# Kernel optimization log

Measured on AMD Instinct MI355X. Metric: run time of the kernel, lower is better.

## Reference

```python
import jax, jax.numpy as jnp
import numpy as np

# Dims (match init_kwargs)
B, N, D_MODEL = 64, 64, 512
D_STATE = 512
D_ATT = D_MODEL
H, W, C, K = 128, 128, 16, 5
T = 32  # num_steps
HALF = K // 2


def _lin(key, out_d, in_d):
    kw, kb = jax.random.split(key)
    w = jax.random.normal(kw, (out_d, in_d), jnp.float32) * 0.02
    b = jax.random.normal(kb, (out_d,), jnp.float32) * 0.02
    return w, b


def setup_inputs() -> dict:
    key = jax.random.key(0)
    ks = jax.random.split(key, 12)
    token_reps = jax.random.normal(ks[0], (B, N, D_MODEL), jnp.float32)
    global_rep = jax.random.normal(ks[1], (B, D_MODEL), jnp.float32)
    attention_mask = jnp.ones((B, N), jnp.int32)
    w_init, b_init = _lin(ks[2], D_STATE, D_MODEL)
    wq, bq = _lin(ks[3], D_ATT, D_STATE)
    wk, bk = _lin(ks[4], D_ATT, D_MODEL)
    wv, bv = _lin(ks[5], D_ATT, D_MODEL)
    gru_in = D_ATT + D_MODEL
    w_ih, b_ih = _lin(ks[6], 3 * D_STATE, gru_in)
    w_hh, b_hh = _lin(ks[7], 3 * D_STATE, D_STATE)
    w_write, b_write = _lin(ks[8], C * K * K, D_STATE + D_ATT)
    w_loc, b_loc = _lin(ks[9], 3, D_STATE + D_ATT + D_MODEL)
    return dict(token_reps=token_reps, global_rep=global_rep, attention_mask=attention_mask,
                w_init=w_init, b_init=b_init, wq=wq, bq=bq, wk=wk, bk=bk, wv=wv, bv=bv,
                w_ih=w_ih, b_ih=b_ih, w_hh=w_hh, b_hh=b_hh,
                w_write=w_write, b_write=b_write, w_loc=w_loc, b_loc=b_loc)


def _forward(token_reps, global_rep, attention_mask,
             w_init, b_init, wq, bq, wk, bk, wv, bv,
             w_ih, b_ih, w_hh, b_hh, w_write, b_write, w_loc, b_loc):
    Bv = token_reps.shape[0]
    # Precompute keys/values (constant over steps)
    k_tok = token_reps @ wk.T + bk  # [B,N,d_att]
    v_tok = token_reps @ wv.T + bv  # [B,N,d_att]
    invalid = attention_mask == 0

    s0 = jnp.tanh(global_rep @ w_init.T + b_init)  # [B,d_state]
    # Padded canvas (NHWC): full KxK patches always fit; crop at the end
    # reproduces the torch clipped-window write exactly.
    canvas0 = jnp.zeros((Bv, H + 2 * HALF, W + 2 * HALF, C), jnp.float32)
    b_idx = jnp.arange(Bv)
    koff = jnp.arange(K)

    def step(carry, _):
        s, canvas_p = carry
        q = s @ wq.T + bq  # [B,d_att]
        scores = jnp.einsum('bd,bnd->bn', q, k_tok)
        scores = jnp.where(invalid, -1e9, scores)
        alpha = jax.nn.softmax(scores, axis=-1)
        r = jnp.einsum('bn,bnd->bd', alpha, v_tok)  # [B,d_att]
        # GRUCell (torch gate order r,z,n)
        x = jnp.concatenate([r, global_rep], axis=-1)
        gi = x @ w_ih.T + b_ih
        gh = s @ w_hh.T + b_hh
        ir, iz, inn = jnp.split(gi, 3, axis=-1)
        hr, hz, hn = jnp.split(gh, 3, axis=-1)
        rg = jax.nn.sigmoid(ir + hr)
        zg = jax.nn.sigmoid(iz + hz)
        ng = jnp.tanh(inn + rg * hn)
        s_new = (1.0 - zg) * ng + zg * s
        # Write patch
        patch = (jnp.concatenate([s_new, r], axis=-1) @ w_write.T + b_write)
        patch = patch.reshape(Bv, C, K, K).transpose(0, 2, 3, 1)  # [B,K,K,C]
        loc = jnp.concatenate([s_new, r, global_rep], axis=-1) @ w_loc.T + b_loc
        cx = jnp.tanh(loc[:, 0])
        cy = jnp.tanh(loc[:, 1])
        j = jnp.clip(jnp.round(0.5 * (cx + 1.0) * (W - 1)), 0, W - 1).astype(jnp.int32)
        i = jnp.clip(jnp.round(0.5 * (cy + 1.0) * (H - 1)), 0, H - 1).astype(jnp.int32)
        # padded coords: top-left of window in padded canvas is (i, j)
        rows = i[:, None] + koff  # [B,K]
        cols = j[:, None] + koff  # [B,K]
        canvas_p = canvas_p.at[b_idx[:, None, None], rows[:, :, None], cols[:, None, :]].add(patch)
        return (s_new, canvas_p), None

    (_, canvas_p), _ = jax.lax.scan(step, (s0, canvas0), None, length=T)
    canvas = canvas_p[:, HALF:HALF + H, HALF:HALF + W, :].transpose(0, 3, 1, 2)  # [B,C,H,W]
    return canvas


def reference(token_reps, global_rep, attention_mask,
              w_init, b_init, wq, bq, wk, bk, wv, bv,
              w_ih, b_ih, w_hh, b_hh, w_write, b_write, w_loc, b_loc):
    return _forward(token_reps, global_rep, attention_mask,
                    w_init, b_init, wq, bq, wk, bk, wv, bv,
                    w_ih, b_ih, w_hh, b_hh, w_write, b_write, w_loc, b_loc)
```

## Files before the change

kernel.cpp:

```cpp
#include <hip/hip_runtime.h>

#define BB 64
#define DD 512
#define TT 32

__device__ __forceinline__ float dot4(const float4 a, const float4 b) {
  return a.x * b.x + a.y * b.y + a.z * b.z + a.w * b.w;
}

__device__ __forceinline__ void cst(float* p, float v) {
  __hip_atomic_store(p, v, __ATOMIC_RELAXED, __HIP_MEMORY_SCOPE_AGENT);
}

__global__ void vecs_k(const float* __restrict__ wq, const float* __restrict__ bk,
                       const float* __restrict__ wk, const float* __restrict__ bq,
                       float* __restrict__ kqb, float* __restrict__ wkbq,
                       float* __restrict__ bqbk, unsigned* __restrict__ bar) {
  const int tid = threadIdx.x, bz = blockIdx.x;
  if (bz < 2) {
    const int d = bz * 256 + tid;
    float s = 0.f;
    for (int e = 0; e < DD; ++e) s += wq[e * DD + d] * bk[e];
    kqb[d] = s;
  } else {
    const int k = (bz - 2) * 256 + tid;
    float s = 0.f;
    for (int e = 0; e < DD; ++e) s += bq[e] * wk[e * DD + k];
    wkbq[k] = s;
    if (bz == 2 && tid == 0) {
      float t2 = 0.f;
      for (int e = 0; e < DD; ++e) t2 += bq[e] * bk[e];
      *bqbk = t2;
    }
    if (bz == 3) {
      if (tid < 16)
        __hip_atomic_store(bar + tid * 64, 0u, __ATOMIC_RELAXED, __HIP_MEMORY_SCOPE_AGENT);
      __hip_atomic_store(bar + 1024 + tid * 32, 0u, __ATOMIC_RELAXED, __HIP_MEMORY_SCOPE_AGENT);
    }
  }
}

__global__ __launch_bounds__(256) void gemm128_k(
    const float* __restrict__ A, int lda, int a_trans,
    const float* __restrict__ B, int ldb, int boff, int b_trans,
    const float* __restrict__ bias, float* __restrict__ C, long c_stride_z, int ldc,
    int kfrom, int klen, int act) {
  __shared__ __align__(16) float As[16][132];
  __shared__ __align__(16) float Bs[16][68];
  const int tid = threadIdx.x;
  const int tx = tid & 15, ty = tid >> 4;
  const int m0 = blockIdx.x * 128, n0 = blockIdx.y * 64;
  const int kbase = kfrom + blockIdx.z * klen;
  float* Ce = C + (long)blockIdx.z * c_stride_z;
  float acc[8][4];
#pragma unroll
  for (int i = 0; i < 8; ++i)
#pragma unroll
    for (int j = 0; j < 4; ++j) acc[i][j] = 0.f;

  for (int k0 = kbase; k0 < kbase + klen; k0 += 16) {
    if (!a_trans) {
      const int row = tid >> 1, half = tid & 1;
      const float* ap = A + (long)(m0 + row) * lda + k0 + half * 8;
      const float4 a0 = *(const float4*)ap;
      const float4 a1 = *(const float4*)(ap + 4);
      const int kb = half * 8;
      As[kb + 0][row] = a0.x; As[kb + 1][row] = a0.y; As[kb + 2][row] = a0.z; As[kb + 3][row] = a0.w;
      As[kb + 4][row] = a1.x; As[kb + 5][row] = a1.y; As[kb + 6][row] = a1.z; As[kb + 7][row] = a1.w;
    } else {
      const int kk = tid >> 4, mseg = tid & 15;
      const float* ap = A + (long)(k0 + kk) * lda + m0 + mseg * 8;
      *(float4*)&As[kk][mseg * 8] = *(const float4*)ap;
      *(float4*)&As[kk][mseg * 8 + 4] = *(const float4*)(ap + 4);
    }
    if (!b_trans) {
      const int n = tid >> 2, q = tid & 3;
      const float4 b0 = *(const float4*)(B + (long)(n0 + n) * ldb + boff + k0 + q * 4);
      Bs[q * 4 + 0][n] = b0.x; Bs[q * 4 + 1][n] = b0.y; Bs[q * 4 + 2][n] = b0.z; Bs[q * 4 + 3][n] = b0.w;
    } else {
      const int kk = tid >> 4, nq = tid & 15;
      *(float4*)&Bs[kk][nq * 4] = *(const float4*)(B + (long)(k0 + kk) * ldb + boff + n0 + nq * 4);
    }
    __syncthreads();
#pragma unroll
    for (int kk = 0; kk < 16; ++kk) {
      const float4 a0 = *(const float4*)&As[kk][ty * 8];
      const float4 a1 = *(const float4*)&As[kk][ty * 8 + 4];
      const float4 b0 = *(const float4*)&Bs[kk][tx * 4];
      const float am[8] = {a0.x, a0.y, a0.z, a0.w, a1.x, a1.y, a1.z, a1.w};
#pragma unroll
      for (int i = 0; i < 8; ++i) {
        acc[i][0] += am[i] * b0.x; acc[i][1] += am[i] * b0.y;
        acc[i][2] += am[i] * b0.z; acc[i][3] += am[i] * b0.w;
      }
    }
    __syncthreads();
  }
  float4 bv = make_float4(0.f, 0.f, 0.f, 0.f);
  if (bias) bv = *(const float4*)(bias + n0 + tx * 4);
#pragma unroll
  for (int i = 0; i < 8; ++i) {
    const int m = m0 + ty * 8 + i;
    float4 v = make_float4(acc[i][0] + bv.x, acc[i][1] + bv.y, acc[i][2] + bv.z, acc[i][3] + bv.w);
    if (act == 1) { v.x = tanhf(v.x); v.y = tanhf(v.y); v.z = tanhf(v.z); v.w = tanhf(v.w); }
    *(float4*)&Ce[(long)m * ldc + n0 + tx * 4] = v;
  }
}

__global__ __launch_bounds__(256) void gemm128_dual_k(
    const float* __restrict__ A,
    const float* __restrict__ B0, const float* __restrict__ bias0, float* __restrict__ C0,
    const float* __restrict__ B1, const float* __restrict__ bias1, float* __restrict__ C1) {
  __shared__ __align__(16) float As[16][132];
  __shared__ __align__(16) float Bs[16][68];
  const int tid = threadIdx.x;
  const int tx = tid & 15, ty = tid >> 4;
  const int m0 = blockIdx.x * 128, n0 = blockIdx.y * 64;
  const float* B = blockIdx.z ? B1 : B0;
  const float* bias = blockIdx.z ? bias1 : bias0;
  float* C = blockIdx.z ? C1 : C0;
  float acc[8][4];
#pragma unroll
  for (int i = 0; i < 8; ++i)
#pragma unroll
    for (int j = 0; j < 4; ++j) acc[i][j] = 0.f;

  for (int k0 = 0; k0 < 512; k0 += 16) {
    {
      const int row = tid >> 1, half = tid & 1;
      const float* ap = A + (long)(m0 + row) * 512 + k0 + half * 8;
      const float4 a0 = *(const float4*)ap;
      const float4 a1 = *(const float4*)(ap + 4);
      const int kb = half * 8;
      As[kb + 0][row] = a0.x; As[kb + 1][row] = a0.y; As[kb + 2][row] = a0.z; As[kb + 3][row] = a0.w;
      As[kb + 4][row] = a1.x; As[kb + 5][row] = a1.y; As[kb + 6][row] = a1.z; As[kb + 7][row] = a1.w;
    }
    {
      const int n = tid >> 2, q = tid & 3;
      const float4 b0 = *(const float4*)(B + (long)(n0 + n) * 512 + k0 + q * 4);
      Bs[q * 4 + 0][n] = b0.x; Bs[q * 4 + 1][n] = b0.y; Bs[q * 4 + 2][n] = b0.z; Bs[q * 4 + 3][n] = b0.w;
    }
    __syncthreads();
#pragma unroll
    for (int kk = 0; kk < 16; ++kk) {
      const float4 a0 = *(const float4*)&As[kk][ty * 8];
      const float4 a1 = *(const float4*)&As[kk][ty * 8 + 4];
      const float4 b0 = *(const float4*)&Bs[kk][tx * 4];
      const float am[8] = {a0.x, a0.y, a0.z, a0.w, a1.x, a1.y, a1.z, a1.w};
#pragma unroll
      for (int i = 0; i < 8; ++i) {
        acc[i][0] += am[i] * b0.x; acc[i][1] += am[i] * b0.y;
        acc[i][2] += am[i] * b0.z; acc[i][3] += am[i] * b0.w;
      }
    }
    __syncthreads();
  }
  const float4 bvv = *(const float4*)(bias + n0 + tx * 4);
#pragma unroll
  for (int i = 0; i < 8; ++i) {
    const int m = m0 + ty * 8 + i;
    float4 v = make_float4(acc[i][0] + bvv.x, acc[i][1] + bvv.y, acc[i][2] + bvv.z, acc[i][3] + bvv.w);
    *(float4*)&C[(long)m * 512 + n0 + tx * 4] = v;
  }
}

__global__ void combine4_k(const float* __restrict__ p, float* __restrict__ out) {
  const int i = blockIdx.x * blockDim.x + threadIdx.x;
  const float4 a = ((const float4*)p)[i];
  const float4 b = ((const float4*)p)[i + 65536];
  const float4 c = ((const float4*)p)[i + 131072];
  const float4 d = ((const float4*)p)[i + 196608];
  ((float4*)out)[i] = make_float4(a.x + b.x + c.x + d.x, a.y + b.y + c.y + d.y,
                                  a.z + b.z + c.z + d.z, a.w + b.w + c.w + d.w);
}

__global__ __launch_bounds__(256) void gemm_k(
    const float* __restrict__ A, int lda, int a_trans,
    const float* __restrict__ B, int ldb, int boff, int b_trans,
    const float* __restrict__ bias,
    float* __restrict__ C, int ldc, int M, int N, int K, int act) {
  __shared__ __align__(16) float As2[32][68];
  __shared__ __align__(16) float Bs2[32][68];
  const int tid = threadIdx.x;
  const int tx = tid & 15, ty = tid >> 4;
  const int m0 = blockIdx.x * 64, n0 = blockIdx.y * 64;
  float acc[4][4] = {};
  for (int k0 = 0; k0 < K; k0 += 32) {
    {
      const int r = tid >> 2, cg2 = (tid & 3) * 8;
      const float* ap = A + (long)(m0 + r) * lda + k0 + cg2;
      const float4 a0 = *(const float4*)ap;
      const float4 a1 = *(const float4*)(ap + 4);
      As2[cg2 + 0][r] = a0.x; As2[cg2 + 1][r] = a0.y; As2[cg2 + 2][r] = a0.z; As2[cg2 + 3][r] = a0.w;
      As2[cg2 + 4][r] = a1.x; As2[cg2 + 5][r] = a1.y; As2[cg2 + 6][r] = a1.z; As2[cg2 + 7][r] = a1.w;
    }
    {
      const int r = tid >> 2, cg2 = (tid & 3) * 8;
      float4 b0 = make_float4(0.f, 0.f, 0.f, 0.f);
      float4 b1 = make_float4(0.f, 0.f, 0.f, 0.f);
      if (n0 + r < N) {
        const float* bp = B + (long)(n0 + r) * ldb + boff + k0 + cg2;
        b0 = *(const float4*)bp;
        b1 = *(const float4*)(bp + 4);
      }
      Bs2[cg2 + 0][r] = b0.x; Bs2[cg2 + 1][r] = b0.y; Bs2[cg2 + 2][r] = b0.z; Bs2[cg2 + 3][r] = b0.w;
      Bs2[cg2 + 4][r] = b1.x; Bs2[cg2 + 5][r] = b1.y; Bs2[cg2 + 6][r] = b1.z; Bs2[cg2 + 7][r] = b1.w;
    }
    __syncthreads();
#pragma unroll
    for (int kk = 0; kk < 32; ++kk) {
      const float4 av = *(const float4*)&As2[kk][ty * 4];
      const float4 bv = *(const float4*)&Bs2[kk][tx * 4];
      acc[0][0] += av.x * bv.x; acc[0][1] += av.x * bv.y; acc[0][2] += av.x * bv.z; acc[0][3] += av.x * bv.w;
      acc[1][0] += av.y * bv.x; acc[1][1] += av.y * bv.y; acc[1][2] += av.y * bv.z; acc[1][3] += av.y * bv.w;
      acc[2][0] += av.z * bv.x; acc[2][1] += av.z * bv.y; acc[2][2] += av.z * bv.z; acc[2][3] += av.z * bv.w;
      acc[3][0] += av.w * bv.x; acc[3][1] += av.w * bv.y; acc[3][2] += av.w * bv.z; acc[3][3] += av.w * bv.w;
    }
    __syncthreads();
  }
#pragma unroll
  for (int i = 0; i < 4; ++i) {
    const int m = m0 + ty * 4 + i;
#pragma unroll
    for (int j = 0; j < 4; ++j) {
      const int n = n0 + tx * 4 + j;
      if (n < N) {
        float v = acc[i][j] + (bias ? bias[n] : 0.f);
        if (act == 1) v = tanhf(v);
        C[(long)m * ldc + n] = v;
      }
    }
  }
}

__device__ __forceinline__ void grid_barrier(unsigned* __restrict__ bar, unsigned gen) {
  __syncthreads();
  const int blk = blockIdx.x, tid = threadIdx.x;
  unsigned* gctr = bar;
  unsigned* rel = bar + 1024;
  if (blk == 0) {
    if (tid == 0)
      __hip_atomic_fetch_add(gctr, 1u, __ATOMIC_RELAXED, __HIP_MEMORY_SCOPE_AGENT);
    if (tid < 16) {
      while (__hip_atomic_load(gctr + tid * 64, __ATOMIC_RELAXED, __HIP_MEMORY_SCOPE_AGENT) < gen * 16u)
        __builtin_amdgcn_s_sleep(1);
    }
    __syncthreads();
    __hip_atomic_store(rel + tid * 32, gen, __ATOMIC_RELAXED, __HIP_MEMORY_SCOPE_AGENT);
  } else {
    if (tid == 0) {
      __hip_atomic_fetch_add(gctr + (blk >> 4) * 64, 1u, __ATOMIC_RELAXED, __HIP_MEMORY_SCOPE_AGENT);
      while (__hip_atomic_load(rel + blk * 32, __ATOMIC_RELAXED, __HIP_MEMORY_SCOPE_AGENT) < gen)
        __builtin_amdgcn_s_sleep(1);
    }
  }
  __syncthreads();
}

__global__ __launch_bounds__(256, 1) void loop_k(
    const float* __restrict__ ktil, const float* __restrict__ cbn,
    const float* __restrict__ vt, const float* __restrict__ locg,
    float* __restrict__ sbuf, float* __restrict__ rbuf,
    const float* __restrict__ w_write, const float* __restrict__ b_write,
    const float* __restrict__ w_loc, const int* __restrict__ amask,
    float* __restrict__ patchbuf, float* __restrict__ locbuf,
    const float* __restrict__ gig, const float* __restrict__ w_ih,
    const float* __restrict__ w_hh, const float* __restrict__ b_hh,
    unsigned* __restrict__ bar) {
  __shared__ __align__(16) float smem[10048];
  __shared__ __align__(16) float wpl[12288];
  float* sm_act = smem;
  float* sm_val = smem + 9216;
  float* sm_sc  = smem + 9408;
  float* sm_s   = smem;
  float* sm_r   = smem + 4608;
  float* sm_g   = smem + 9216;

  const int blk = blockIdx.x, tid = threadIdx.x, lane = tid & 63;
  const bool is_attn = (blk < 64);
  const bool is_patch = (blk >= 64) && (blk < 224);
  unsigned nsync = 0;

  int p_rg = 0, p_bg = 0;
  if (is_patch) {
    const int g = blk - 64;
    p_bg = g & 3; p_rg = g >> 2;
    for (int idx = tid; idx < 3072; idx += 256) {
      const int rho = idx >> 8, f4 = idx & 255;
      const int col = f4 << 2;
      const int cc2 = col >> 5, jj = (col >> 2) & 7;
      const int dcol = (cc2 << 5) | ((jj ^ (cc2 & 7)) << 2);
      const float* src = (rho < 10) ? (w_write + (long)(p_rg * 10 + rho) * 1024 + col)
                                    : (w_loc + (long)(rho - 10) * 1536 + col);
      *(float4*)(wpl + rho * 1024 + dcol) = *(const float4*)src;
    }
  }

  float4 wg[3][8];
  const int g_dg = blk & 63, g_bg = blk >> 6;
  {
    const int c = tid & 15, sl = tid >> 4;
#pragma unroll
    for (int i = 0; i < 3; ++i) {
      const int rho = sl * 3 + i;
      const float* wsrc;
      if (rho < 24) {
        const int g2 = rho >> 3, di = rho & 7;
        wsrc = w_ih + (long)(g2 * 512 + g_dg * 8 + di) * 1024 + c * 32;
      } else {
        const int rh = rho - 24, g2 = rh >> 3, di = rh & 7;
        wsrc = w_hh + (long)(g2 * 512 + g_dg * 8 + di) * 512 + c * 32;
      }
#pragma unroll
      for (int j = 0; j < 8; ++j) wg[i][j] = *(const float4*)(wsrc + 4 * j);
    }
  }
  __syncthreads();

  for (int t = 0; t <= TT; ++t) {
    const float* s_cur = sbuf + (long)t * (BB * DD);
    float* r_cur = rbuf + (long)t * (BB * DD);
    const float* r_prev = r_cur - BB * DD;

    if (is_attn) {
      if (t < TT) {
        const int b = blk, wrp = tid >> 6;
        const float* sb = s_cur + (long)b * DD;
        const float4 sva = *(const float4*)(sb + lane * 8);
        const float4 svb = *(const float4*)(sb + lane * 8 + 4);
        for (int h8 = 0; h8 < 2; ++h8) {
          const float* kbase = ktil + ((long)(b * 64 + wrp * 16 + h8 * 8)) * DD + lane * 8;
          float4 ka[8], kb2[8];
#pragma unroll
          for (int i = 0; i < 8; ++i) {
            ka[i] = *(const float4*)(kbase + (long)i * DD);
            kb2[i] = *(const float4*)(kbase + (long)i * DD + 4);
          }
#pragma unroll
          for (int i = 0; i < 8; ++i) {
            float p = dot4(ka[i], sva) + dot4(kb2[i], svb);
#pragma unroll
            for (int off = 32; off; off >>= 1) p += __shfl_xor(p, off);
            if (lane == 0) {
              const int n = wrp * 16 + h8 * 8 + i;
              float sc = p + cbn[b * 64 + n];
              if (amask[b * 64 + n] == 0) sc = -1e9f;
              sm_sc[n] = sc;
            }
          }
        }
        __syncthreads();
        if (tid < 64) {
          const float v = sm_sc[tid];
          float m = v;
#pragma unroll
          for (int off = 32; off; off >>= 1) m = fmaxf(m, __shfl_xor(m, off));
          const float e = expf(v - m);
          float l2 = e;
#pragma unroll
          for (int off = 32; off; off >>= 1) l2 += __shfl_xor(l2, off);
          sm_sc[tid] = e / l2;
        }
        __syncthreads();
        float rx = 0.f, ry = 0.f;
        const float* vb = vt + (long)b * 64 * DD + (tid << 1);
        for (int n0 = 0; n0 < 64; n0 += 8) {
          float2 vv[8];
#pragma unroll
          for (int i = 0; i < 8; ++i)
            vv[i] = *(const float2*)(vb + (long)(n0 + i) * DD);
#pragma unroll
          for (int i = 0; i < 8; ++i) {
            const float a = sm_sc[n0 + i];
            rx = fmaf(a, vv[i].x, rx);
            ry = fmaf(a, vv[i].y, ry);
          }
        }
        cst(r_cur + (long)b * DD + (tid << 1), rx);
        cst(r_cur + (long)b * DD + (tid << 1) + 1, ry);
      }
    } else if (is_patch) {
      if (t >= 1) {
        const int c = tid & 31, sl = tid >> 5;
        const int tr = sl & 3, bgsub = sl >> 2;
        for (int h = 0; h < 2; ++h) {
          __syncthreads();
          {
            const int b_i8 = tid >> 5, l = tid & 31;
            const int b = p_bg * 16 + h * 8 + b_i8;
            const float* sp = s_cur + (long)b * DD + l * 16;
            const float* rp = r_prev + (long)b * DD + l * 16;
            float* dsd = sm_act + b_i8 * 1152 + (l >> 1) * 36 + (l & 1) * 16;
            float* drd = sm_act + b_i8 * 1152 + (16 + (l >> 1)) * 36 + (l & 1) * 16;
#pragma unroll
            for (int jj = 0; jj < 4; ++jj) {
              *(float4*)(dsd + 4 * jj) = *(const float4*)(sp + 4 * jj);
              *(float4*)(drd + 4 * jj) = *(const float4*)(rp + 4 * jj);
            }
          }
          __syncthreads();
          float4 wreg[3][8];
#pragma unroll
          for (int i = 0; i < 3; ++i) {
            const float* wrow = wpl + (tr * 3 + i) * 1024 + (c << 5);
#pragma unroll
            for (int j = 0; j < 8; ++j)
              wreg[i][j] = *(const float4*)(wrow + ((j ^ (c & 7)) << 2));
          }
          for (int bi = 0; bi < 4; ++bi) {
            const int bl = bgsub * 4 + bi;
            const int babs = p_bg * 16 + h * 8 + bl;
            const float* ap = sm_act + bl * 1152 + c * 36;
            float a0 = 0.f, a1 = 0.f, a2 = 0.f;
#pragma unroll
            for (int j = 0; j < 8; ++j) {
              const float4 av = *(const float4*)(ap + 4 * j);
              a0 += dot4(wreg[0][j], av);
              a1 += dot4(wreg[1][j], av);
              a2 += dot4(wreg[2][j], av);
            }
#pragma unroll
            for (int m = 1; m < 32; m <<= 1) {
              a0 += __shfl_xor(a0, m);
              a1 += __shfl_xor(a1, m);
              a2 += __shfl_xor(a2, m);
            }
            if (c == 0) {
              const int bslot = h * 8 + bl;
              const float av3[3] = {a0, a1, a2};
#pragma unroll
              for (int i = 0; i < 3; ++i) {
                const int rho = tr * 3 + i;
                float v = av3[i];
                if (rho >= 10) v += locg[babs * 2 + (rho - 10)];
                sm_val[rho * 16 + bslot] = v;
              }
            }
          }
        }
        __syncthreads();
        const int u = t - 1;
        if (tid < 160) {
          const int ri = tid >> 4, bl2 = tid & 15;
          const int row = p_rg * 10 + ri;
          const int b = p_bg * 16 + bl2;
          patchbuf[((long)u * 64 + b) * 400 + row] = sm_val[ri * 16 + bl2] + b_write[row];
        }
        if (p_rg == 0 && tid < 16) {
          const int b = p_bg * 16 + tid;
          const float lx = sm_val[160 + tid];
          const float ly = sm_val[176 + tid];
          const int jx = min(127, max(0, (int)rintf(0.5f * (tanhf(lx) + 1.f) * 127.f)));
          const int iy = min(127, max(0, (int)rintf(0.5f * (tanhf(ly) + 1.f) * 127.f)));
          locbuf[((long)u * 64 + b) * 2] = (float)jx;
          locbuf[((long)u * 64 + b) * 2 + 1] = (float)iy;
        }
      }
    }

    if (t == TT) break;

    grid_barrier(bar, ++nsync);

    {
      float* s_nxt = sbuf + (long)(t + 1) * (BB * DD);
      const int c = tid & 15, sl = tid >> 4;
      for (int h = 0; h < 2; ++h) {
        __syncthreads();
        {
          const int b_i8 = tid >> 5, l = tid & 31;
          const int b = g_bg * 16 + h * 8 + b_i8;
          const float* sp = s_cur + (long)b * DD + l * 16;
          const float* rp = r_cur + (long)b * DD + l * 16;
          float* dsd = sm_s + b_i8 * 576 + (l >> 1) * 36 + (l & 1) * 16;
          float* drd = sm_r + b_i8 * 576 + (l >> 1) * 36 + (l & 1) * 16;
#pragma unroll
          for (int jj = 0; jj < 4; ++jj) {
            *(float4*)(dsd + 4 * jj) = *(const float4*)(sp + 4 * jj);
            *(float4*)(drd + 4 * jj) = *(const float4*)(rp + 4 * jj);
          }
        }
        __syncthreads();
        const float* base = (sl < 8) ? sm_r : sm_s;
        for (int bl = 0; bl < 8; ++bl) {
          const float* ap = base + bl * 576 + c * 36;
          float a0 = 0.f, a1 = 0.f, a2 = 0.f;
#pragma unroll
          for (int j = 0; j < 8; ++j) {
            const float4 av = *(const float4*)(ap + 4 * j);
            a0 += dot4(wg[0][j], av);
            a1 += dot4(wg[1][j], av);
            a2 += dot4(wg[2][j], av);
          }
#pragma unroll
          for (int m = 1; m < 16; m <<= 1) {
            a0 += __shfl_xor(a0, m);
            a1 += __shfl_xor(a1, m);
            a2 += __shfl_xor(a2, m);
          }
          if (c == 0) {
            const int bslot = h * 8 + bl;
            sm_g[bslot * 52 + sl * 3 + 0] = a0;
            sm_g[bslot * 52 + sl * 3 + 1] = a1;
            sm_g[bslot * 52 + sl * 3 + 2] = a2;
          }
        }
      }
      __syncthreads();
      if (tid < 128) {
        const int b_i = tid >> 3, di = tid & 7;
        const int b = g_bg * 16 + b_i, d = g_dg * 8 + di;
        const float ir = sm_g[b_i * 52 + di]        + gig[b * 1536 + d];
        const float iz = sm_g[b_i * 52 + 8 + di]    + gig[b * 1536 + 512 + d];
        const float in = sm_g[b_i * 52 + 16 + di]   + gig[b * 1536 + 1024 + d];
        const float hr = sm_g[b_i * 52 + 24 + di]   + b_hh[d];
        const float hz = sm_g[b_i * 52 + 32 + di]   + b_hh[512 + d];
        const float hn = sm_g[b_i * 52 + 40 + di]   + b_hh[1024 + d];
        const float rg2 = 1.f / (1.f + expf(-(ir + hr)));
        const float zg = 1.f / (1.f + expf(-(iz + hz)));
        const float ng = tanhf(in + rg2 * hn);
        const float sprev = s_cur[(long)b * DD + d];
        cst(s_nxt + (long)b * DD + d, (1.f - zg) * ng + zg * sprev);
      }
    }

    grid_barrier(bar, ++nsync);
  }
}

__global__ __launch_bounds__(256) void canvas_k(const float* __restrict__ pb,
                                                const float* __restrict__ lb,
                                                float* __restrict__ canvas) {
  __shared__ float ch[16384];
  const int blk = blockIdx.x, tid = threadIdx.x;
  const int b = blk >> 4, c = blk & 15;
  for (int i = tid; i < 4096; i += 256)
    ((float4*)ch)[i] = make_float4(0.f, 0.f, 0.f, 0.f);
  __syncthreads();
  for (int u = 0; u < TT; ++u) {
    const int jx = (int)lb[((long)u * 64 + b) * 2];
    const int iy = (int)lb[((long)u * 64 + b) * 2 + 1];
    if (tid < 25) {
      const float v = pb[((long)u * 64 + b) * 400 + c * 25 + tid];
      const int ki = tid / 5, kj = tid % 5;
      const int y = iy + ki - 2, x = jx + kj - 2;
      if (y >= 0 && y < 128 && x >= 0 && x < 128) ch[y * 128 + x] += v;
    }
    __syncthreads();
  }
  float* dst = canvas + ((long)b * 16 + c) * 16384;
  for (int i = tid; i < 4096; i += 256)
    ((float4*)dst)[i] = ((float4*)ch)[i];
}

extern "C" void kernel_launch(void* const* d_in, const int* in_sizes, int n_in,
                              void* d_out, int out_size, void* d_ws, size_t ws_size,
                              hipStream_t stream) {
  const float* tok     = (const float*)d_in[0];
  const float* grep    = (const float*)d_in[1];
  const int*   amask   = (const int*)d_in[2];
  const float* w_init  = (const float*)d_in[3];
  const float* b_init  = (const float*)d_in[4];
  const float* wq      = (const float*)d_in[5];
  const float* bq      = (const float*)d_in[6];
  const float* wk      = (const float*)d_in[7];
  const float* bk      = (const float*)d_in[8];
  const float* wv      = (const float*)d_in[9];
  const float* bv      = (const float*)d_in[10];
  const float* w_ih    = (const float*)d_in[11];
  const float* b_ih    = (const float*)d_in[12];
  const float* w_hh    = (const float*)d_in[13];
  const float* b_hh    = (const float*)d_in[14];
  const float* w_write = (const float*)d_in[15];
  const float* b_write = (const float*)d_in[16];
  const float* w_loc   = (const float*)d_in[17];
  const float* b_loc   = (const float*)d_in[18];
  float* canvas = (float*)d_out;

  float* ws = (float*)d_ws;
  float* ktil = ws;
  float* vtw  = ktil + 2097152;
  float* Aqk  = vtw + 2097152;
  float* gig  = Aqk + 262144;
  float* cbn  = gig + 98304;
  float* sbuf = cbn + 4096;
  float* rbuf = sbuf + 1081344;
  float* locg = rbuf + 1048576;
  float* kqb  = locg + 128;
  float* wkbq = kqb + 512;
  float* bqbk = wkbq + 512;
  unsigned* bar = (unsigned*)(bqbk + 64);
  float* patchbuf = (float*)(bar + 16384);
  float* locbuf = patchbuf + 819200;

  vecs_k<<<4, 256, 0, stream>>>(wq, bk, wk, bq, kqb, wkbq, bqbk, bar);
  gemm128_k<<<dim3(4, 8, 4), 256, 0, stream>>>(wq, 512, 1, wk, 512, 0, 1,
                                               nullptr, vtw, 262144L, 512, 0, 128, 0);
  combine4_k<<<256, 256, 0, stream>>>(vtw, Aqk);
  gemm128_dual_k<<<dim3(32, 8, 2), 256, 0, stream>>>(tok, Aqk, kqb, ktil, wv, bv, vtw);
  gemm_k<<<dim3(64, 1), 256, 0, stream>>>(tok, 512, 0, wkbq, 0, 0, 0, bqbk, cbn, 1, 4096, 1, 512, 0);
  gemm_k<<<dim3(1, 24), 256, 0, stream>>>(grep, 512, 0, w_ih, 1024, 512, 0, b_ih, gig, 1536, 64, 1536, 512, 0);
  gemm_k<<<dim3(1, 8), 256, 0, stream>>>(grep, 512, 0, w_init, 512, 0, 0, b_init, sbuf, 512, 64, 512, 512, 1);
  gemm_k<<<dim3(1, 1), 256, 0, stream>>>(grep, 512, 0, w_loc, 1536, 1024, 0, b_loc, locg, 2, 64, 2, 512, 0);

  loop_k<<<256, 256, 0, stream>>>(ktil, cbn, vtw, locg, sbuf, rbuf, w_write, b_write,
                                  w_loc, amask, patchbuf, locbuf, gig, w_ih, w_hh, b_hh, bar);
  canvas_k<<<1024, 256, 0, stream>>>(patchbuf, locbuf, canvas);
}
```

Baseline: 1.158 ms.

## Replace grid-wide barrier with per-pod barriers over independent batch groups

The persistent loop kernel is reorganised so that each group of 64 blocks (a pod) owns 16 batch rows, covering their attention, patch and GRU work. The global two-level barrier is replaced by a flat per-pod barrier: each block writes its generation to a slot and one wavefront polls all 64 slots with a wave vote. This aims to cut barrier latency and contention, since pods never need to wait for each other. It depends on the data flow within each step being confined to a single batch group, and it changes how work is mapped to blocks.

```diff
diff --git a/kernel.cpp b/kernel.cpp
--- a/kernel.cpp
+++ b/kernel.cpp
@@ -33,9 +33,8 @@
       *bqbk = t2;
     }
     if (bz == 3) {
-      if (tid < 16)
-        __hip_atomic_store(bar + tid * 64, 0u, __ATOMIC_RELAXED, __HIP_MEMORY_SCOPE_AGENT);
-      __hip_atomic_store(bar + 1024 + tid * 32, 0u, __ATOMIC_RELAXED, __HIP_MEMORY_SCOPE_AGENT);
+      __hip_atomic_store(bar + tid, 0u, __ATOMIC_RELAXED, __HIP_MEMORY_SCOPE_AGENT);
+      __hip_atomic_store(bar + 256 + tid, 0u, __ATOMIC_RELAXED, __HIP_MEMORY_SCOPE_AGENT);
     }
   }
 }
@@ -233,25 +232,16 @@
   }
 }
 
-__device__ __forceinline__ void grid_barrier(unsigned* __restrict__ bar, unsigned gen) {
+__device__ __forceinline__ void pod_barrier(unsigned* __restrict__ arr, int local, unsigned gen) {
   __syncthreads();
-  const int blk = blockIdx.x, tid = threadIdx.x;
-  unsigned* gctr = bar;
-  unsigned* rel = bar + 1024;
-  if (blk == 0) {
-    if (tid == 0)
-      __hip_atomic_fetch_add(gctr, 1u, __ATOMIC_RELAXED, __HIP_MEMORY_SCOPE_AGENT);
-    if (tid < 16) {
-      while (__hip_atomic_load(gctr + tid * 64, __ATOMIC_RELAXED, __HIP_MEMORY_SCOPE_AGENT) < gen * 16u)
-        __builtin_amdgcn_s_sleep(1);
-    }
-    __syncthreads();
-    __hip_atomic_store(rel + tid * 32, gen, __ATOMIC_RELAXED, __HIP_MEMORY_SCOPE_AGENT);
-  } else {
-    if (tid == 0) {
-      __hip_atomic_fetch_add(gctr + (blk >> 4) * 64, 1u, __ATOMIC_RELAXED, __HIP_MEMORY_SCOPE_AGENT);
-      while (__hip_atomic_load(rel + blk * 32, __ATOMIC_RELAXED, __HIP_MEMORY_SCOPE_AGENT) < gen)
-        __builtin_amdgcn_s_sleep(1);
+  const int tid = threadIdx.x;
+  if (tid == 0)
+    __hip_atomic_store(arr + local, gen, __ATOMIC_RELAXED, __HIP_MEMORY_SCOPE_AGENT);
+  if (tid < 64) {
+    for (;;) {
+      const unsigned v = __hip_atomic_load(arr + tid, __ATOMIC_RELAXED, __HIP_MEMORY_SCOPE_AGENT);
+      if (__all(v >= gen)) break;
+      __builtin_amdgcn_s_sleep(1);
     }
   }
   __syncthreads();
@@ -277,14 +267,17 @@
   float* sm_g   = smem + 9216;
 
   const int blk = blockIdx.x, tid = threadIdx.x, lane = tid & 63;
-  const bool is_attn = (blk < 64);
-  const bool is_patch = (blk >= 64) && (blk < 224);
+  const int pod = blk >> 6, local = blk & 63;
+  unsigned* arr = bar + pod * 128;
+  const bool is_attn = (local < 16);
+  const bool is_patch = (local >= 16) && (local < 56);
+  const int ab = pod * 16 + local;
   unsigned nsync = 0;
 
-  int p_rg = 0, p_bg = 0;
+  int p_rg = 0;
+  const int p_bg = pod;
   if (is_patch) {
-    const int g = blk - 64;
-    p_bg = g & 3; p_rg = g >> 2;
+    p_rg = local - 16;
     for (int idx = tid; idx < 3072; idx += 256) {
       const int rho = idx >> 8, f4 = idx & 255;
       const int col = f4 << 2;
@@ -297,7 +290,7 @@
   }
 
   float4 wg[3][8];
-  const int g_dg = blk & 63, g_bg = blk >> 6;
+  const int g_dg = local, g_bg = pod;
   {
     const int c = tid & 15, sl = tid >> 4;
 #pragma unroll
@@ -324,7 +317,7 @@
 
     if (is_attn) {
       if (t < TT) {
-        const int b = blk, wrp = tid >> 6;
+        const int b = ab, wrp = tid >> 6;
         const float* sb = s_cur + (long)b * DD;
         const float4 sva = *(const float4*)(sb + lane * 8);
         const float4 svb = *(const float4*)(sb + lane * 8 + 4);
@@ -460,7 +453,7 @@
 
     if (t == TT) break;
 
-    grid_barrier(bar, ++nsync);
+    pod_barrier(arr, local, ++nsync);
 
     {
       float* s_nxt = sbuf + (long)(t + 1) * (BB * DD);
@@ -524,7 +517,7 @@
       }
     }
 
-    grid_barrier(bar, ++nsync);
+    pod_barrier(arr, local, ++nsync);
   }
 }
 
```

New measurement: 1.260 ms. 8.8% more time.

## Fold small prologue GEMMs into persistent loop kernel before first grid barrier

Applied to the files above, without the earlier changes.

Removes four small gemm_k launches (mask-bias vector, global-rep input gates, initial state with tanh, location bias) and computes them inside loop_k's first blocks, followed by a grid barrier replacing the local syncthreads. The aim is to cut launch overhead and poorly-utilised tiny GEMM launches. In exchange it adds one extra grid-wide barrier, and those blocks do serial dot-product work before the barrier while the others wait.

```diff
diff --git a/kernel.cpp b/kernel.cpp
--- a/kernel.cpp
+++ b/kernel.cpp
@@ -174,65 +174,6 @@
                                   a.z + b.z + c.z + d.z, a.w + b.w + c.w + d.w);
 }
 
-__global__ __launch_bounds__(256) void gemm_k(
-    const float* __restrict__ A, int lda, int a_trans,
-    const float* __restrict__ B, int ldb, int boff, int b_trans,
-    const float* __restrict__ bias,
-    float* __restrict__ C, int ldc, int M, int N, int K, int act) {
-  __shared__ __align__(16) float As2[32][68];
-  __shared__ __align__(16) float Bs2[32][68];
-  const int tid = threadIdx.x;
-  const int tx = tid & 15, ty = tid >> 4;
-  const int m0 = blockIdx.x * 64, n0 = blockIdx.y * 64;
-  float acc[4][4] = {};
-  for (int k0 = 0; k0 < K; k0 += 32) {
-    {
-      const int r = tid >> 2, cg2 = (tid & 3) * 8;
-      const float* ap = A + (long)(m0 + r) * lda + k0 + cg2;
-      const float4 a0 = *(const float4*)ap;
-      const float4 a1 = *(const float4*)(ap + 4);
-      As2[cg2 + 0][r] = a0.x; As2[cg2 + 1][r] = a0.y; As2[cg2 + 2][r] = a0.z; As2[cg2 + 3][r] = a0.w;
-      As2[cg2 + 4][r] = a1.x; As2[cg2 + 5][r] = a1.y; As2[cg2 + 6][r] = a1.z; As2[cg2 + 7][r] = a1.w;
-    }
-    {
-      const int r = tid >> 2, cg2 = (tid & 3) * 8;
-      float4 b0 = make_float4(0.f, 0.f, 0.f, 0.f);
-      float4 b1 = make_float4(0.f, 0.f, 0.f, 0.f);
-      if (n0 + r < N) {
-        const float* bp = B + (long)(n0 + r) * ldb + boff + k0 + cg2;
-        b0 = *(const float4*)bp;
-        b1 = *(const float4*)(bp + 4);
-      }
-      Bs2[cg2 + 0][r] = b0.x; Bs2[cg2 + 1][r] = b0.y; Bs2[cg2 + 2][r] = b0.z; Bs2[cg2 + 3][r] = b0.w;
-      Bs2[cg2 + 4][r] = b1.x; Bs2[cg2 + 5][r] = b1.y; Bs2[cg2 + 6][r] = b1.z; Bs2[cg2 + 7][r] = b1.w;
-    }
-    __syncthreads();
-#pragma unroll
-    for (int kk = 0; kk < 32; ++kk) {
-      const float4 av = *(const float4*)&As2[kk][ty * 4];
-      const float4 bv = *(const float4*)&Bs2[kk][tx * 4];
-      acc[0][0] += av.x * bv.x; acc[0][1] += av.x * bv.y; acc[0][2] += av.x * bv.z; acc[0][3] += av.x * bv.w;
-      acc[1][0] += av.y * bv.x; acc[1][1] += av.y * bv.y; acc[1][2] += av.y * bv.z; acc[1][3] += av.y * bv.w;
-      acc[2][0] += av.z * bv.x; acc[2][1] += av.z * bv.y; acc[2][2] += av.z * bv.z; acc[2][3] += av.z * bv.w;
-      acc[3][0] += av.w * bv.x; acc[3][1] += av.w * bv.y; acc[3][2] += av.w * bv.z; acc[3][3] += av.w * bv.w;
-    }
-    __syncthreads();
-  }
-#pragma unroll
-  for (int i = 0; i < 4; ++i) {
-    const int m = m0 + ty * 4 + i;
-#pragma unroll
-    for (int j = 0; j < 4; ++j) {
-      const int n = n0 + tx * 4 + j;
-      if (n < N) {
-        float v = acc[i][j] + (bias ? bias[n] : 0.f);
-        if (act == 1) v = tanhf(v);
-        C[(long)m * ldc + n] = v;
-      }
-    }
-  }
-}
-
 __device__ __forceinline__ void grid_barrier(unsigned* __restrict__ bar, unsigned gen) {
   __syncthreads();
   const int blk = blockIdx.x, tid = threadIdx.x;
@@ -258,15 +199,19 @@
 }
 
 __global__ __launch_bounds__(256, 1) void loop_k(
-    const float* __restrict__ ktil, const float* __restrict__ cbn,
-    const float* __restrict__ vt, const float* __restrict__ locg,
+    const float* __restrict__ ktil, float* __restrict__ cbn,
+    const float* __restrict__ vt, float* __restrict__ locg,
     float* __restrict__ sbuf, float* __restrict__ rbuf,
     const float* __restrict__ w_write, const float* __restrict__ b_write,
     const float* __restrict__ w_loc, const int* __restrict__ amask,
     float* __restrict__ patchbuf, float* __restrict__ locbuf,
-    const float* __restrict__ gig, const float* __restrict__ w_ih,
+    float* __restrict__ gig, const float* __restrict__ w_ih,
     const float* __restrict__ w_hh, const float* __restrict__ b_hh,
-    unsigned* __restrict__ bar) {
+    unsigned* __restrict__ bar,
+    const float* __restrict__ tok, const float* __restrict__ grep,
+    const float* __restrict__ wkbq, const float* __restrict__ bqbk,
+    const float* __restrict__ w_init, const float* __restrict__ b_init,
+    const float* __restrict__ b_ih, const float* __restrict__ b_loc) {
   __shared__ __align__(16) float smem[10048];
   __shared__ __align__(16) float wpl[12288];
   float* sm_act = smem;
@@ -280,6 +225,64 @@
   const bool is_attn = (blk < 64);
   const bool is_patch = (blk >= 64) && (blk < 224);
   unsigned nsync = 0;
+
+  if (blk < 16) {
+    for (int i = tid; i < 512; i += 256) smem[i] = wkbq[i];
+    __syncthreads();
+    const int m = blk * 256 + tid;
+    const float* tr = tok + (long)m * 512;
+    float acc = bqbk[0];
+    for (int e = 0; e < 512; e += 8) {
+      acc += dot4(*(const float4*)(tr + e), *(const float4*)(smem + e));
+      acc += dot4(*(const float4*)(tr + e + 4), *(const float4*)(smem + e + 4));
+    }
+    cst(cbn + m, acc);
+    __syncthreads();
+  } else if (blk < 40) {
+    const int o = (blk - 16) * 64 + (tid & 63);
+    const int b0 = (tid >> 6) * 16;
+    float acc[16];
+#pragma unroll
+    for (int i = 0; i < 16; ++i) acc[i] = 0.f;
+    const float* wr = w_ih + (long)o * 1024 + 512;
+    for (int e = 0; e < 512; e += 4) {
+      const float4 w4 = *(const float4*)(wr + e);
+#pragma unroll
+      for (int i = 0; i < 16; ++i)
+        acc[i] += dot4(*(const float4*)(grep + (long)(b0 + i) * 512 + e), w4);
+    }
+    const float bi = b_ih[o];
+#pragma unroll
+    for (int i = 0; i < 16; ++i)
+      cst(gig + (long)(b0 + i) * 1536 + o, acc[i] + bi);
+  } else if (blk < 48) {
+    const int d = (blk - 40) * 64 + (tid & 63);
+    const int b0 = (tid >> 6) * 16;
+    float acc[16];
+#pragma unroll
+    for (int i = 0; i < 16; ++i) acc[i] = 0.f;
+    const float* wr = w_init + (long)d * 512;
+    for (int e = 0; e < 512; e += 4) {
+      const float4 w4 = *(const float4*)(wr + e);
+#pragma unroll
+      for (int i = 0; i < 16; ++i)
+        acc[i] += dot4(*(const float4*)(grep + (long)(b0 + i) * 512 + e), w4);
+    }
+    const float bi = b_init[d];
+#pragma unroll
+    for (int i = 0; i < 16; ++i)
+      cst(sbuf + (long)(b0 + i) * 512 + d, tanhf(acc[i] + bi));
+  } else if (blk == 48) {
+    if (tid < 128) {
+      const int b = tid >> 1, j = tid & 1;
+      const float* wr = w_loc + (long)j * 1536 + 1024;
+      const float* gr = grep + (long)b * 512;
+      float acc = b_loc[j];
+      for (int e = 0; e < 512; e += 4)
+        acc += dot4(*(const float4*)(gr + e), *(const float4*)(wr + e));
+      cst(locg + b * 2 + j, acc);
+    }
+  }
 
   int p_rg = 0, p_bg = 0;
   if (is_patch) {
@@ -315,7 +318,8 @@
       for (int j = 0; j < 8; ++j) wg[i][j] = *(const float4*)(wsrc + 4 * j);
     }
   }
-  __syncthreads();
+
+  grid_barrier(bar, ++nsync);
 
   for (int t = 0; t <= TT; ++t) {
     const float* s_cur = sbuf + (long)t * (BB * DD);
@@ -598,12 +602,9 @@
                                                nullptr, vtw, 262144L, 512, 0, 128, 0);
   combine4_k<<<256, 256, 0, stream>>>(vtw, Aqk);
   gemm128_dual_k<<<dim3(32, 8, 2), 256, 0, stream>>>(tok, Aqk, kqb, ktil, wv, bv, vtw);
-  gemm_k<<<dim3(64, 1), 256, 0, stream>>>(tok, 512, 0, wkbq, 0, 0, 0, bqbk, cbn, 1, 4096, 1, 512, 0);
-  gemm_k<<<dim3(1, 24), 256, 0, stream>>>(grep, 512, 0, w_ih, 1024, 512, 0, b_ih, gig, 1536, 64, 1536, 512, 0);
-  gemm_k<<<dim3(1, 8), 256, 0, stream>>>(grep, 512, 0, w_init, 512, 0, 0, b_init, sbuf, 512, 64, 512, 512, 1);
-  gemm_k<<<dim3(1, 1), 256, 0, stream>>>(grep, 512, 0, w_loc, 1536, 1024, 0, b_loc, locg, 2, 64, 2, 512, 0);
 
   loop_k<<<256, 256, 0, stream>>>(ktil, cbn, vtw, locg, sbuf, rbuf, w_write, b_write,
-                                  w_loc, amask, patchbuf, locbuf, gig, w_ih, w_hh, b_hh, bar);
+                                  w_loc, amask, patchbuf, locbuf, gig, w_ih, w_hh, b_hh, bar,
+                                  tok, grep, wkbq, bqbk, w_init, b_init, b_ih, b_loc);
   canvas_k<<<1024, 256, 0, stream>>>(patchbuf, locbuf, canvas);
 }
```

New measurement: 1.107 ms. -4.4%, faster.
